# Kernel tuning notes

Measured on AMD Instinct MI355X. Metric: run time of the kernel, lower is better.

Reference implementation:

```python
import jax, jax.numpy as jnp
import numpy as np

L_KLD, L_ROOT, L_DISP, L_CONS, L_FK = 0.001, 1.0, 1.0, 0.1, 0.1


def quat_mul(a, b):
    # w-first Hamilton product, broadcasting over leading dims
    aw, ax, ay, az = a[..., 0], a[..., 1], a[..., 2], a[..., 3]
    bw, bx, by, bz = b[..., 0], b[..., 1], b[..., 2], b[..., 3]
    return jnp.stack([
        aw * bw - ax * bx - ay * by - az * bz,
        aw * bx + ax * bw + ay * bz - az * by,
        aw * by - ax * bz + ay * bw + az * bx,
        aw * bz + ax * by - ay * bx + az * bw,
    ], axis=-1)


def quat_inv(q):
    conj = q * jnp.array([1.0, -1.0, -1.0, -1.0], q.dtype)
    return conj / jnp.sum(q * q, axis=-1, keepdims=True)


def quat_rotate(q, v):
    # rotate vector v by quaternion q: q * (0, v) * q^-1
    q, vb = jnp.broadcast_arrays(q[..., :1], v[..., :1])  # shape probe
    qv = jnp.concatenate([jnp.zeros_like(v[..., :1]), v], axis=-1)
    return quat_mul(quat_mul(jnp.broadcast_to(jnp.asarray(0.0), ()).astype(qv.dtype) * 0 + 1 and None or None, qv), quat_inv(qv))  # placeholder


# clean implementation (the above placeholder is unused)
def quat_rotate(q, v):  # noqa: F811
    qv = jnp.concatenate([jnp.zeros_like(v[..., :1]), v], axis=-1)
    return quat_mul(quat_mul(q, qv), quat_inv(q))[..., 1:]


def from_root_quat(q, parents):
    # q: [..., J, 4] root-relative quats -> local quats.
    # Vectorized form of the reversed per-joint loop: parents are read
    # before being modified (parent < j), so a single gather is exact.
    qp = jnp.take(q, parents, axis=-2)
    loc = quat_mul(quat_inv(qp), q)
    keep = (parents == 0)[:, None]  # joints whose parent is root keep q
    return jnp.where(keep, q, loc)


def fk(local, offsets, parents):
    # local: [Bp,2,T,J,4]; offsets: [Bp,1,1,J,3]; returns global positions [Bp,2,T,J,3]
    J = local.shape[-2]
    grot = jnp.zeros_like(local).at[..., 0, :].set(local[..., 0, :])
    gpos = jnp.zeros(local.shape[:-1] + (3,), local.dtype)
    for j in range(1, J):  # fixed small structural loop over skeleton joints
        p = parents[j]
        pr = jnp.take(grot, p, axis=-2)  # parent global rotation [Bp,2,T,4]
        pp = jnp.take(gpos, p, axis=-2)  # parent global position [Bp,2,T,3]
        grot = grot.at[..., j, :].set(quat_mul(pr, local[..., j, :]))
        gpos = gpos.at[..., j, :].set(pp + quat_rotate(pr, offsets[..., j, :]))
    return gpos


def mse(a, b):
    return jnp.mean((a - b) ** 2)


def reference(base_motion, target_motion, input_displacement, target_displacement,
              mu, logvar, latent, W_dec, mean_q, std_q, offsets, parents):
    Bp, _, C, T = base_motion.shape
    J = C // 4
    Z = latent.shape[-1]
    offs = offsets[:, None, None, :, :]  # [Bp,1,1,J,3] (tile over pair dim via broadcast)
    root_id = jnp.array([1.0, 0.0, 0.0, 0.0], base_motion.dtype)[:, None]  # (4,1)

    def decode(lat):
        # input_motion is the decoder output in the original training loop
        m = jnp.einsum('pkz,zc->pkc', lat.reshape(Bp, 2, Z), W_dec)
        return base_motion + m.reshape(Bp, 2, C, T)

    def motion_to_pos(qs):
        qs = qs * std_q + mean_q
        qs = qs.at[..., :4, :].set(root_id)  # root quat -> identity
        q = qs.transpose(0, 1, 3, 2).reshape(Bp, 2, T, J, 4)
        return fk(from_root_quat(q, parents), offs, parents)

    # quaternion part of target dual quaternions
    target_qs = target_motion.reshape(Bp, 2, J, 8, T)[:, :, :, :4, :].reshape(Bp, 2, C, T)

    qs = decode(latent)
    loss_joints = mse(qs[..., 4:, :], target_qs[..., 4:, :])
    loss_root = mse(qs[..., :4, :], target_qs[..., :4, :])

    pos_from_lat = lambda lat: motion_to_pos(decode(lat))
    pos_qs = pos_from_lat(latent)
    pos_target = motion_to_pos(target_qs)
    loss_fk = mse(pos_qs, pos_target)

    loss_disp = mse(input_displacement, target_displacement)
    loss_kld = -0.5 * jnp.mean(jnp.sum(1.0 + logvar - mu ** 2 - jnp.exp(logvar), axis=-1))

    # drag consistency: grad of sum_p ||pos_p0 - pos_p1||^2 w.r.t. latent
    def f_sum(lat):
        pos = pos_from_lat(lat)
        return jnp.sum((pos[:, 0] - pos[:, 1]) ** 2)

    grad_f = jax.grad(f_sum)(latent)
    lp = latent.reshape(Bp, 2, Z)
    z_drag = lp[:, 0] - grad_f.reshape(Bp, 2, Z)[:, 0]
    loss_cons = mse(z_drag, lp[:, 1])

    # order: kld, root, displacement, consecutive, fk, joints
    return jnp.stack([loss_kld * L_KLD, loss_root * L_ROOT, loss_disp * L_DISP,
                      loss_cons * L_CONS, loss_fk * L_FK, loss_joints])


def setup_inputs() -> dict:
    key = jax.random.key(0)
    ks = jax.random.split(key, 11)
    Bp, C, T, J, Z = 512, 96, 128, 24, 256
    parents = jnp.array(np.array(
        [0, 0, 0, 0, 1, 2, 3, 4, 5, 6, 7, 8, 9, 9, 9, 12, 13, 14, 16, 17, 18, 19, 20, 21],
        dtype=np.int32))
    return {
        'base_motion': jax.random.normal(ks[0], (Bp, 2, C, T), jnp.float32),
        'target_motion': jax.random.normal(ks[1], (Bp, 2, 2 * C, T), jnp.float32),
        'input_displacement': jax.random.normal(ks[2], (Bp, 2, 3, T), jnp.float32),
        'target_displacement': jax.random.normal(ks[3], (Bp, 2, 3, T), jnp.float32),
        'mu': jax.random.normal(ks[4], (2 * Bp, Z), jnp.float32),
        'logvar': 0.1 * jax.random.normal(ks[5], (2 * Bp, Z), jnp.float32),
        'latent': jax.random.normal(ks[6], (2 * Bp, Z), jnp.float32),
        'W_dec': 0.02 * jax.random.normal(ks[7], (Z, C * T), jnp.float32),
        'mean_q': 0.1 * jax.random.normal(ks[8], (C, 1), jnp.float32),
        'std_q': jax.random.uniform(ks[9], (C, 1), jnp.float32, 0.5, 1.5),
        'offsets': 0.1 * jax.random.normal(ks[10], (Bp, J, 3), jnp.float32),
        'parents': parents,
    }
```

## Files before the change

kernel.cpp:

```cpp
#include <hip/hip_runtime.h>
#include <utility>

#define DEVI __device__ __forceinline__

namespace {

constexpr int T_ = 128;
constexpr int NCH = 96;
constexpr int CT = NCH * T_;
constexpr int NJ = 24;
constexpr int ZDIM = 256;
constexpr int PAR[NJ] = {0,0,0,0,1,2,3,4,5,6,7,8,9,9,9,12,13,14,16,17,18,19,20,21};

struct Q  { float w,x,y,z; };
struct V3 { float x,y,z; };

DEVI Q qmul(Q a, Q b){
  return Q{ a.w*b.w - a.x*b.x - a.y*b.y - a.z*b.z,
            a.w*b.x + a.x*b.w + a.y*b.z - a.z*b.y,
            a.w*b.y - a.x*b.z + a.y*b.w + a.z*b.x,
            a.w*b.z + a.x*b.y - a.y*b.x + a.z*b.w };
}
DEVI Q qconj(Q a){ return Q{a.w,-a.x,-a.y,-a.z}; }
DEVI float qn2(Q a){ return a.w*a.w + a.x*a.x + a.y*a.y + a.z*a.z; }
DEVI Q qscale(Q a, float s){ return Q{a.w*s, a.x*s, a.y*s, a.z*s}; }
DEVI Q qadd(Q a, Q b){ return Q{a.w+b.w, a.x+b.x, a.y+b.y, a.z+b.z}; }
DEVI Q qinv(Q a){ return qscale(qconj(a), 1.0f/qn2(a)); }
DEVI V3 qrot(Q g, V3 v){
  Q t = qmul(g, Q{0.f, v.x, v.y, v.z});
  Q y = qmul(t, qconj(g));
  float in = 1.0f/qn2(g);
  return V3{y.x*in, y.y*in, y.z*in};
}
DEVI Q qinv_bwd(Q q, Q g){
  float n  = qn2(q);
  float in = 1.0f/n;
  float d  = g.w*q.w - g.x*q.x - g.y*q.y - g.z*q.z;
  float c  = 2.0f*d*in*in;
  return Q{ g.w*in - q.w*c, -g.x*in - q.x*c, -g.y*in - q.y*c, -g.z*in - q.z*c };
}
DEVI Q qrot_bwd_g(Q g, V3 v, V3 w){
  float in = 1.0f/qn2(g);
  Q u{0.f, v.x, v.y, v.z};
  Q t = qmul(g, u);
  Q y = qmul(t, qconj(g));
  Q G4{0.f, w.x*in, w.y*in, w.z*in};
  Q dt  = qmul(G4, g);
  Q dcg = qmul(qconj(t), G4);
  Q dg  = qconj(dcg);
  dg = qadd(dg, qmul(dt, qconj(u)));
  float wy = w.x*y.x + w.y*y.y + w.z*y.z;
  dg = qadd(dg, qscale(g, -2.0f*wy*in*in));
  return dg;
}

template<typename F, int... Is>
DEVI void sf_impl(F&& f, std::integer_sequence<int, Is...>){
  (f(std::integral_constant<int, Is>{}), ...);
}
template<int N, typename F>
DEVI void static_for(F&& f){ sf_impl(f, std::make_integer_sequence<int, N>{}); }

template<int Jj>
DEVI Q loadQ(const float (&q)[NJ][4]){ return Q{q[Jj][0], q[Jj][1], q[Jj][2], q[Jj][3]}; }
template<int Jj>
DEVI Q localQ(const float (&q)[NJ][4]){
  if constexpr (Jj < 4) return loadQ<Jj>(q);
  else return qmul(qinv(loadQ<PAR[Jj]>(q)), loadQ<Jj>(q));
}
template<int Jj>
DEVI Q grotRec(const float (&q)[NJ][4]){
  if constexpr (Jj == 0) return Q{1.f,0.f,0.f,0.f};
  else return qmul(grotRec<PAR[Jj]>(q), localQ<Jj>(q));
}

template<bool TGT, typename PJ>
DEVI void chainFwd(const float* __restrict__ base, int t,
                   const float* s_std, const float* s_mean, const float* s_off,
                   float (&q)[NJ][4], PJ&& pj)
{
  Q grot[NJ]; V3 gpos[NJ];
  static_for<NJ>([&](auto jc){
    constexpr int j = decltype(jc)::value;
    if constexpr (j == 0) {
      q[0][0]=1.f; q[0][1]=0.f; q[0][2]=0.f; q[0][3]=0.f;
      grot[0] = Q{1.f,0.f,0.f,0.f};
      gpos[0] = V3{0.f,0.f,0.f};
    } else {
      constexpr int P = PAR[j];
      #pragma unroll
      for (int i = 0; i < 4; ++i){
        const int c  = 4*j + i;
        const int oc = TGT ? (8*j + i) : c;
        q[j][i] = base[oc*T_ + t] * s_std[c] + s_mean[c];
      }
      Q qj{q[j][0], q[j][1], q[j][2], q[j][3]};
      Q L;
      if constexpr (j < 4) L = qj;
      else L = qmul(qinv(Q{q[P][0], q[P][1], q[P][2], q[P][3]}), qj);
      Q gP = grot[P];
      grot[j] = qmul(gP, L);
      V3 o{s_off[3*j], s_off[3*j+1], s_off[3*j+2]};
      V3 r = qrot(gP, o);
      gpos[j] = V3{gpos[P].x + r.x, gpos[P].y + r.y, gpos[P].z + r.z};
    }
    pj(jc, gpos[j]);
  });
}

DEVI void chainBwd(const float (&q)[NJ][4], const float* s_std, const float* s_off,
                   V3 (&dgp)[NJ], float* __restrict__ Gp, int t)
{
  Q dgr[NJ] = {};
  Q dq [NJ] = {};
  static_for<NJ-1>([&](auto ic){
    constexpr int j = NJ - 1 - decltype(ic)::value;
    constexpr int P = PAR[j];
    V3 w = dgp[j];
    Q gP = grotRec<P>(q);
    if constexpr (P != 0) {
      dgp[P].x += w.x; dgp[P].y += w.y; dgp[P].z += w.z;
      V3 o{s_off[3*j], s_off[3*j+1], s_off[3*j+2]};
      dgr[P] = qadd(dgr[P], qrot_bwd_g(gP, o, w));
    }
    Q Gj = dgr[j];
    Q dL = qmul(qconj(gP), Gj);
    if constexpr (P != 0) {
      dgr[P] = qadd(dgr[P], qmul(Gj, qconj(localQ<j>(q))));
    }
    if constexpr (j < 4) {
      dq[j] = qadd(dq[j], dL);
    } else {
      Q qP  = loadQ<P>(q);
      Q iqP = qinv(qP);
      dq[j] = qadd(dq[j], qmul(qconj(iqP), dL));
      Q dInv = qmul(dL, qconj(loadQ<j>(q)));
      dq[P] = qadd(dq[P], qinv_bwd(qP, dInv));
    }
    Gp[(4*j+0)*T_ + t] = dq[j].w * s_std[4*j+0];
    Gp[(4*j+1)*T_ + t] = dq[j].x * s_std[4*j+1];
    Gp[(4*j+2)*T_ + t] = dq[j].y * s_std[4*j+2];
    Gp[(4*j+3)*T_ + t] = dq[j].z * s_std[4*j+3];
  });
  #pragma unroll
  for (int i = 0; i < 4; ++i) Gp[i*T_ + t] = 0.f;
}

DEVI float waveSum(float v){
  #pragma unroll
  for (int o = 32; o > 0; o >>= 1) v += __shfl_down(v, o);
  return v;
}

}


__global__ __launch_bounds__(256) void k_decode(
    const float* __restrict__ base, const float* __restrict__ lat,
    const float* __restrict__ W, float* __restrict__ qs)
{
  __shared__ float As[32][132];
  __shared__ float Bs[32][128];
  const int tid = threadIdx.x;
  const int bn = blockIdx.x * 128;
  const int bm = blockIdx.y * 128;
  float acc[8][8] = {};
  for (int k0 = 0; k0 < 256; k0 += 32) {
    #pragma unroll
    for (int r = 0; r < 4; ++r) {
      int idx = r*256 + tid;
      int row = idx >> 3;
      int kc  = (idx & 7) << 2;
      float4 v = *(const float4*)&lat[(size_t)(bm + row)*256 + k0 + kc];
      As[kc+0][row] = v.x; As[kc+1][row] = v.y;
      As[kc+2][row] = v.z; As[kc+3][row] = v.w;
    }
    #pragma unroll
    for (int r = 0; r < 4; ++r) {
      int idx = r*256 + tid;
      int kr = idx >> 5;
      int nc = (idx & 31) << 2;
      *(float4*)&Bs[kr][nc] = *(const float4*)&W[(size_t)(k0 + kr)*CT + bn + nc];
    }
    __syncthreads();
    const int tx = tid & 15, ty = tid >> 4;
    #pragma unroll
    for (int kk = 0; kk < 32; ++kk) {
      float a[8], b[8];
      float4 a0 = *(float4*)&As[kk][ty*8];
      float4 a1 = *(float4*)&As[kk][ty*8+4];
      float4 b0 = *(float4*)&Bs[kk][tx*8];
      float4 b1 = *(float4*)&Bs[kk][tx*8+4];
      a[0]=a0.x;a[1]=a0.y;a[2]=a0.z;a[3]=a0.w;a[4]=a1.x;a[5]=a1.y;a[6]=a1.z;a[7]=a1.w;
      b[0]=b0.x;b[1]=b0.y;b[2]=b0.z;b[3]=b0.w;b[4]=b1.x;b[5]=b1.y;b[6]=b1.z;b[7]=b1.w;
      #pragma unroll
      for (int i = 0; i < 8; ++i)
        #pragma unroll
        for (int j = 0; j < 8; ++j) acc[i][j] += a[i]*b[j];
    }
    __syncthreads();
  }
  const int tx = tid & 15, ty = tid >> 4;
  #pragma unroll
  for (int i = 0; i < 8; ++i) {
    size_t row = bm + ty*8 + i;
    #pragma unroll
    for (int j = 0; j < 8; j += 4) {
      size_t col = bn + tx*8 + j;
      float4 bv = *(const float4*)&base[row*CT + col];
      float4 o;
      o.x = bv.x + acc[i][j+0]; o.y = bv.y + acc[i][j+1];
      o.z = bv.z + acc[i][j+2]; o.w = bv.w + acc[i][j+3];
      *(float4*)&qs[row*CT + col] = o;
    }
  }
}

__global__ __launch_bounds__(128, 1) void k_pose(
    const float* __restrict__ qs,   const float* __restrict__ tmot,
    const float* __restrict__ meanq,const float* __restrict__ stdq,
    const float* __restrict__ offs, float* __restrict__ G,
    float* __restrict__ bpose)
{
  __shared__ float s_std[96], s_mean[96], s_off[72];
  __shared__ float sred[3][2];
  const int p = blockIdx.x;
  const int t = threadIdx.x;
  if (t < 96) { s_std[t] = stdq[t]; s_mean[t] = meanq[t]; }
  if (t < 72) s_off[t] = offs[p*72 + t];
  __syncthreads();

  const float* qs0 = qs   + (size_t)(2*p) * CT;
  const float* qs1 = qs0  + CT;
  const float* tm0 = tmot + (size_t)(2*p) * (2*CT);
  const float* tm1 = tm0  + 2*CT;

  float accR = 0.f, accJ = 0.f;
  #pragma unroll 4
  for (int c = 0; c < 4; ++c) {
    int oc = ((c >> 2) << 3) + (c & 3);
    float d0 = qs0[c*T_ + t] - tm0[oc*T_ + t];
    float d1 = qs1[c*T_ + t] - tm1[oc*T_ + t];
    accR += d0*d0 + d1*d1;
  }
  #pragma unroll 4
  for (int c = 4; c < 96; ++c) {
    int oc = ((c >> 2) << 3) + (c & 3);
    float d0 = qs0[c*T_ + t] - tm0[oc*T_ + t];
    float d1 = qs1[c*T_ + t] - tm1[oc*T_ + t];
    accJ += d0*d0 + d1*d1;
  }

  float fkAcc = 0.f;
  V3 posA[NJ], posB[NJ];
  float qtmp[NJ][4], qd0[NJ][4];

  chainFwd<true >(tm0, t, s_std, s_mean, s_off, qtmp,
    [&](auto jc, V3 g){ posA[decltype(jc)::value] = g; });
  chainFwd<false>(qs0, t, s_std, s_mean, s_off, qd0,
    [&](auto jc, V3 g){
      constexpr int j = decltype(jc)::value;
      float dx = g.x - posA[j].x, dy = g.y - posA[j].y, dz = g.z - posA[j].z;
      fkAcc += dx*dx + dy*dy + dz*dz;
      posB[j] = g;
    });
  chainFwd<true >(tm1, t, s_std, s_mean, s_off, qtmp,
    [&](auto jc, V3 g){ posA[decltype(jc)::value] = g; });
  V3 dgp[NJ];
  chainFwd<false>(qs1, t, s_std, s_mean, s_off, qtmp,
    [&](auto jc, V3 g){
      constexpr int j = decltype(jc)::value;
      float dx = g.x - posA[j].x, dy = g.y - posA[j].y, dz = g.z - posA[j].z;
      fkAcc += dx*dx + dy*dy + dz*dz;
      dgp[j] = V3{2.f*(posB[j].x - g.x), 2.f*(posB[j].y - g.y), 2.f*(posB[j].z - g.z)};
    });

  chainBwd(qd0, s_std, s_off, dgp, G + (size_t)p * CT, t);

  float r  = waveSum(accR);
  float jj = waveSum(accJ);
  float fk = waveSum(fkAcc);
  const int wid = t >> 6;
  if ((t & 63) == 0) { sred[0][wid] = r; sred[1][wid] = jj; sred[2][wid] = fk; }
  __syncthreads();
  if (t == 0) {
    bpose[p]        = sred[0][0] + sred[0][1];
    bpose[512 + p]  = sred[1][0] + sred[1][1];
    bpose[1024 + p] = sred[2][0] + sred[2][1];
  }
}

__global__ __launch_bounds__(256) void k_gradgemm(
    const float* __restrict__ G, const float* __restrict__ W,
    float* __restrict__ part)
{
  __shared__ float As[64][33];
  __shared__ float Bs[128][33];
  const int tid = threadIdx.x;
  const int bn = blockIdx.x * 128;
  const int bm = blockIdx.y * 64;
  const int s  = blockIdx.z;
  const int kb = s * 768;
  float acc[4][8] = {};
  for (int k0 = 0; k0 < 768; k0 += 32) {
    #pragma unroll
    for (int r = 0; r < 2; ++r) {
      int idx = r*256 + tid;
      int row = idx >> 3;
      int kc  = (idx & 7) << 2;
      float4 v = *(const float4*)&G[(size_t)(bm + row)*CT + kb + k0 + kc];
      As[row][kc+0]=v.x; As[row][kc+1]=v.y; As[row][kc+2]=v.z; As[row][kc+3]=v.w;
    }
    #pragma unroll
    for (int r = 0; r < 4; ++r) {
      int idx = r*256 + tid;
      int row = idx >> 3;
      int kc  = (idx & 7) << 2;
      float4 v = *(const float4*)&W[(size_t)(bn + row)*CT + kb + k0 + kc];
      Bs[row][kc+0]=v.x; Bs[row][kc+1]=v.y; Bs[row][kc+2]=v.z; Bs[row][kc+3]=v.w;
    }
    __syncthreads();
    const int tx = tid & 15, ty = tid >> 4;
    #pragma unroll
    for (int kk = 0; kk < 32; ++kk) {
      float a[4], b[8];
      #pragma unroll
      for (int i = 0; i < 4; ++i) a[i] = As[ty*4+i][kk];
      #pragma unroll
      for (int j = 0; j < 8; ++j) b[j] = Bs[tx*8+j][kk];
      #pragma unroll
      for (int i = 0; i < 4; ++i)
        #pragma unroll
        for (int j = 0; j < 8; ++j) acc[i][j] += a[i]*b[j];
    }
    __syncthreads();
  }
  const int tx = tid & 15, ty = tid >> 4;
  #pragma unroll
  for (int i = 0; i < 4; ++i) {
    size_t pr = (size_t)s*131072 + (size_t)(bm + ty*4 + i)*256 + bn + tx*8;
    float4 o0{acc[i][0], acc[i][1], acc[i][2], acc[i][3]};
    float4 o1{acc[i][4], acc[i][5], acc[i][6], acc[i][7]};
    *(float4*)&part[pr]   = o0;
    *(float4*)&part[pr+4] = o1;
  }
}

__global__ __launch_bounds__(256) void k_rest(
    const float* __restrict__ ind, const float* __restrict__ tgd,
    const float* __restrict__ mu,  const float* __restrict__ lv,
    const float* __restrict__ lat, const float* __restrict__ part,
    float* __restrict__ brest)
{
  __shared__ float sred[3][4];
  const int t = threadIdx.x;
  const int gid = blockIdx.x * 256 + t;
  float a0 = 0.f, a1 = 0.f, a2 = 0.f;
  if (gid < 98304) {
    float4 a = ((const float4*)ind)[gid];
    float4 b = ((const float4*)tgd)[gid];
    float dx=a.x-b.x, dy=a.y-b.y, dz=a.z-b.z, dw=a.w-b.w;
    a0 = dx*dx + dy*dy + dz*dz + dw*dw;
  }
  if (gid < 65536) {
    float4 l = ((const float4*)lv)[gid];
    float4 m = ((const float4*)mu)[gid];
    a1 = (1.f + l.x - m.x*m.x - __expf(l.x)) + (1.f + l.y - m.y*m.y - __expf(l.y))
       + (1.f + l.z - m.z*m.z - __expf(l.z)) + (1.f + l.w - m.w*m.w - __expf(l.w));
  }
  if (gid < 32768) {
    float4 g{0.f,0.f,0.f,0.f};
    #pragma unroll
    for (int s = 0; s < 16; ++s) {
      float4 v = ((const float4*)(part + (size_t)s*131072))[gid];
      g.x += v.x; g.y += v.y; g.z += v.z; g.w += v.w;
    }
    int p  = gid >> 6;
    int zb = (gid & 63) << 2;
    float4 La = *(const float4*)&lat[(size_t)(2*p)*ZDIM + zb];
    float4 Lb = *(const float4*)&lat[(size_t)(2*p+1)*ZDIM + zb];
    float vx = La.x - g.x - Lb.x, vy = La.y - g.y - Lb.y;
    float vz = La.z - g.z - Lb.z, vw = La.w - g.w - Lb.w;
    a2 = vx*vx + vy*vy + vz*vz + vw*vw;
  }
  a0 = waveSum(a0); a1 = waveSum(a1); a2 = waveSum(a2);
  const int wid = t >> 6;
  if ((t & 63) == 0) { sred[0][wid]=a0; sred[1][wid]=a1; sred[2][wid]=a2; }
  __syncthreads();
  if (t == 0) {
    brest[blockIdx.x]        = sred[0][0]+sred[0][1]+sred[0][2]+sred[0][3];
    brest[512 + blockIdx.x]  = sred[1][0]+sred[1][1]+sred[1][2]+sred[1][3];
    brest[1024 + blockIdx.x] = sred[2][0]+sred[2][1]+sred[2][2]+sred[2][3];
  }
}

__global__ __launch_bounds__(256) void k_final(
    const float* __restrict__ bpose, const float* __restrict__ brest,
    float* __restrict__ out)
{
  __shared__ float sred[4];
  const int t = threadIdx.x;
  float tot[6];
  const float* srcs[6] = { bpose, bpose+512, bpose+1024, brest, brest+512, brest+1024 };
  #pragma unroll
  for (int c = 0; c < 6; ++c) {
    float x = srcs[c][t] + srcs[c][t+256];
    x = waveSum(x);
    if ((t & 63) == 0) sred[t>>6] = x;
    __syncthreads();
    tot[c] = sred[0]+sred[1]+sred[2]+sred[3];
    __syncthreads();
  }
  if (t == 0) {
    out[0] = 0.001f * (-0.5f * tot[4] * (1.f/1024.f));
    out[1] = tot[0] * (1.f/524288.f);
    out[2] = tot[3] * (1.f/393216.f);
    out[3] = 0.1f * (tot[5] * (1.f/131072.f));
    out[4] = 0.1f * (tot[2] * (1.f/9437184.f));
    out[5] = tot[1] * (1.f/12058624.f);
  }
}

extern "C" void kernel_launch(void* const* d_in, const int* in_sizes, int n_in,
                              void* d_out, int out_size, void* d_ws, size_t ws_size,
                              hipStream_t stream)
{
  (void)in_sizes; (void)n_in; (void)out_size; (void)ws_size;
  const float* base = (const float*)d_in[0];
  const float* tmot = (const float*)d_in[1];
  const float* ind  = (const float*)d_in[2];
  const float* tgd  = (const float*)d_in[3];
  const float* mu   = (const float*)d_in[4];
  const float* lv   = (const float*)d_in[5];
  const float* lat  = (const float*)d_in[6];
  const float* W    = (const float*)d_in[7];
  const float* meanq= (const float*)d_in[8];
  const float* stdq = (const float*)d_in[9];
  const float* offs = (const float*)d_in[10];
  float* out = (float*)d_out;

  char* ws = (char*)d_ws;
  float* qs    = (float*)(ws);
  float* G     = (float*)(ws + 50331648);
  float* part  = (float*)(ws + 75497472);
  float* bpose = (float*)(ws + 83886080);
  float* brest = (float*)(ws + 83892224);

  hipLaunchKernelGGL(k_decode,   dim3(96, 8),    dim3(256), 0, stream, base, lat, W, qs);
  hipLaunchKernelGGL(k_pose,     dim3(512),      dim3(128), 0, stream, qs, tmot, meanq, stdq, offs, G, bpose);
  hipLaunchKernelGGL(k_gradgemm, dim3(2, 8, 16), dim3(256), 0, stream, G, W, part);
  hipLaunchKernelGGL(k_rest,     dim3(512),      dim3(256), 0, stream, ind, tgd, mu, lv, lat, part, brest);
  hipLaunchKernelGGL(k_final,    dim3(1),        dim3(256), 0, stream, bpose, brest, out);
}
```

Before: 479.9 us.

## Split pose kernel into forward and backward passes with stored global rotations

The fused pose kernel is split into a forward kernel and a backward kernel. The forward kernel writes the per-joint global rotations and the position gradients to workspace. The backward kernel reads them back instead of recomputing parent global rotations inside the reverse chain loop. This is meant to cut register pressure and redundant quaternion recomputation, at the cost of extra global memory traffic and an added launch. The new path runs only when the workspace is large enough; otherwise the original fused kernel is used.

Result: slower. 505.8 us (+5.4%).

```diff
diff --git a/kernel.cpp b/kernel.cpp
--- a/kernel.cpp
+++ b/kernel.cpp
@@ -108,6 +108,41 @@
   });
 }
 
+template<bool TGT, typename PJ>
+DEVI void chainFwdG(const float* __restrict__ base, int t,
+                    const float* s_std, const float* s_mean, const float* s_off,
+                    PJ&& pj)
+{
+  float q[NJ][4];
+  Q grot[NJ]; V3 gpos[NJ];
+  static_for<NJ>([&](auto jc){
+    constexpr int j = decltype(jc)::value;
+    if constexpr (j == 0) {
+      q[0][0]=1.f; q[0][1]=0.f; q[0][2]=0.f; q[0][3]=0.f;
+      grot[0] = Q{1.f,0.f,0.f,0.f};
+      gpos[0] = V3{0.f,0.f,0.f};
+    } else {
+      constexpr int P = PAR[j];
+      #pragma unroll
+      for (int i = 0; i < 4; ++i){
+        const int c  = 4*j + i;
+        const int oc = TGT ? (8*j + i) : c;
+        q[j][i] = base[oc*T_ + t] * s_std[c] + s_mean[c];
+      }
+      Q qj{q[j][0], q[j][1], q[j][2], q[j][3]};
+      Q L;
+      if constexpr (j < 4) L = qj;
+      else L = qmul(qinv(Q{q[P][0], q[P][1], q[P][2], q[P][3]}), qj);
+      Q gP = grot[P];
+      grot[j] = qmul(gP, L);
+      V3 o{s_off[3*j], s_off[3*j+1], s_off[3*j+2]};
+      V3 r = qrot(gP, o);
+      gpos[j] = V3{gpos[P].x + r.x, gpos[P].y + r.y, gpos[P].z + r.z};
+    }
+    pj(jc, gpos[j], grot[j]);
+  });
+}
+
 DEVI void chainBwd(const float (&q)[NJ][4], const float* s_std, const float* s_off,
                    V3 (&dgp)[NJ], float* __restrict__ Gp, int t)
 {
@@ -290,6 +325,158 @@
   }
 }
 
+__global__ __launch_bounds__(128) void k_pose_fwd(
+    const float* __restrict__ qs,   const float* __restrict__ tmot,
+    const float* __restrict__ meanq,const float* __restrict__ stdq,
+    const float* __restrict__ offs, float* __restrict__ grot_ws,
+    float* __restrict__ dgp_ws,     float* __restrict__ bpose)
+{
+  __shared__ float s_std[96], s_mean[96], s_off[72];
+  __shared__ float sred[3][2];
+  const int p = blockIdx.x;
+  const int t = threadIdx.x;
+  if (t < 96) { s_std[t] = stdq[t]; s_mean[t] = meanq[t]; }
+  if (t < 72) s_off[t] = offs[p*72 + t];
+  __syncthreads();
+
+  const float* qs0 = qs   + (size_t)(2*p) * CT;
+  const float* qs1 = qs0  + CT;
+  const float* tm0 = tmot + (size_t)(2*p) * (2*CT);
+  const float* tm1 = tm0  + 2*CT;
+
+  float accR = 0.f, accJ = 0.f;
+  #pragma unroll 4
+  for (int c = 0; c < 4; ++c) {
+    int oc = ((c >> 2) << 3) + (c & 3);
+    float d0 = qs0[c*T_ + t] - tm0[oc*T_ + t];
+    float d1 = qs1[c*T_ + t] - tm1[oc*T_ + t];
+    accR += d0*d0 + d1*d1;
+  }
+  #pragma unroll 4
+  for (int c = 4; c < 96; ++c) {
+    int oc = ((c >> 2) << 3) + (c & 3);
+    float d0 = qs0[c*T_ + t] - tm0[oc*T_ + t];
+    float d1 = qs1[c*T_ + t] - tm1[oc*T_ + t];
+    accJ += d0*d0 + d1*d1;
+  }
+
+  float fkAcc = 0.f;
+  V3 posA[NJ], posB[NJ];
+  float* gw = grot_ws + (size_t)p * (NJ*4*T_);
+  float* dw = dgp_ws  + (size_t)p * (NJ*3*T_);
+
+  chainFwdG<true >(tm0, t, s_std, s_mean, s_off,
+    [&](auto jc, V3 g, Q gr){ posA[decltype(jc)::value] = g; (void)gr; });
+  chainFwdG<false>(qs0, t, s_std, s_mean, s_off,
+    [&](auto jc, V3 g, Q gr){
+      constexpr int j = decltype(jc)::value;
+      float dx = g.x - posA[j].x, dy = g.y - posA[j].y, dz = g.z - posA[j].z;
+      fkAcc += dx*dx + dy*dy + dz*dz;
+      posB[j] = g;
+      if constexpr (j >= 1) {
+        gw[(j*4+0)*T_ + t] = gr.w; gw[(j*4+1)*T_ + t] = gr.x;
+        gw[(j*4+2)*T_ + t] = gr.y; gw[(j*4+3)*T_ + t] = gr.z;
+      }
+    });
+  chainFwdG<true >(tm1, t, s_std, s_mean, s_off,
+    [&](auto jc, V3 g, Q gr){ posA[decltype(jc)::value] = g; (void)gr; });
+  chainFwdG<false>(qs1, t, s_std, s_mean, s_off,
+    [&](auto jc, V3 g, Q gr){
+      constexpr int j = decltype(jc)::value;
+      float dx = g.x - posA[j].x, dy = g.y - posA[j].y, dz = g.z - posA[j].z;
+      fkAcc += dx*dx + dy*dy + dz*dz;
+      (void)gr;
+      if constexpr (j >= 1) {
+        dw[(j*3+0)*T_ + t] = 2.f*(posB[j].x - g.x);
+        dw[(j*3+1)*T_ + t] = 2.f*(posB[j].y - g.y);
+        dw[(j*3+2)*T_ + t] = 2.f*(posB[j].z - g.z);
+      }
+    });
+
+  float r  = waveSum(accR);
+  float jj = waveSum(accJ);
+  float fk = waveSum(fkAcc);
+  const int wid = t >> 6;
+  if ((t & 63) == 0) { sred[0][wid] = r; sred[1][wid] = jj; sred[2][wid] = fk; }
+  __syncthreads();
+  if (t == 0) {
+    bpose[p]        = sred[0][0] + sred[0][1];
+    bpose[512 + p]  = sred[1][0] + sred[1][1];
+    bpose[1024 + p] = sred[2][0] + sred[2][1];
+  }
+}
+
+__global__ __launch_bounds__(128) void k_pose_bwd(
+    const float* __restrict__ qs,   const float* __restrict__ meanq,
+    const float* __restrict__ stdq, const float* __restrict__ offs,
+    const float* __restrict__ grot_ws, const float* __restrict__ dgp_ws,
+    float* __restrict__ G)
+{
+  __shared__ float s_std[96], s_mean[96], s_off[72];
+  const int p = blockIdx.x;
+  const int t = threadIdx.x;
+  if (t < 96) { s_std[t] = stdq[t]; s_mean[t] = meanq[t]; }
+  if (t < 72) s_off[t] = offs[p*72 + t];
+  __syncthreads();
+
+  const float* qs0 = qs + (size_t)(2*p) * CT;
+  const float* gw  = grot_ws + (size_t)p * (NJ*4*T_);
+  const float* dw  = dgp_ws  + (size_t)p * (NJ*3*T_);
+  float* Gp = G + (size_t)p * CT;
+
+  float q[NJ][4];
+  q[0][0]=1.f; q[0][1]=0.f; q[0][2]=0.f; q[0][3]=0.f;
+  static_for<NJ-1>([&](auto jc){
+    constexpr int j = decltype(jc)::value + 1;
+    #pragma unroll
+    for (int i = 0; i < 4; ++i) {
+      const int c = 4*j + i;
+      q[j][i] = qs0[c*T_ + t] * s_std[c] + s_mean[c];
+    }
+  });
+
+  V3 dgpacc[NJ] = {};
+  Q dgr[NJ] = {};
+  Q dq [NJ] = {};
+  static_for<NJ-1>([&](auto ic){
+    constexpr int j = NJ - 1 - decltype(ic)::value;
+    constexpr int P = PAR[j];
+    V3 w{ dw[(j*3+0)*T_ + t] + dgpacc[j].x,
+          dw[(j*3+1)*T_ + t] + dgpacc[j].y,
+          dw[(j*3+2)*T_ + t] + dgpacc[j].z };
+    Q gP;
+    if constexpr (P == 0) gP = Q{1.f,0.f,0.f,0.f};
+    else gP = Q{ gw[(P*4+0)*T_ + t], gw[(P*4+1)*T_ + t],
+                 gw[(P*4+2)*T_ + t], gw[(P*4+3)*T_ + t] };
+    if constexpr (P != 0) {
+      dgpacc[P].x += w.x; dgpacc[P].y += w.y; dgpacc[P].z += w.z;
+      V3 o{s_off[3*j], s_off[3*j+1], s_off[3*j+2]};
+      dgr[P] = qadd(dgr[P], qrot_bwd_g(gP, o, w));
+    }
+    Q Gj = dgr[j];
+    Q dL = qmul(qconj(gP), Gj);
+    if constexpr (P != 0) {
+      Q localj = qmul(qinv(loadQ<P>(q)), loadQ<j>(q));
+      dgr[P] = qadd(dgr[P], qmul(Gj, qconj(localj)));
+    }
+    if constexpr (j < 4) {
+      dq[j] = qadd(dq[j], dL);
+    } else {
+      Q qP  = loadQ<P>(q);
+      Q iqP = qinv(qP);
+      dq[j] = qadd(dq[j], qmul(qconj(iqP), dL));
+      Q dInv = qmul(dL, qconj(loadQ<j>(q)));
+      dq[P] = qadd(dq[P], qinv_bwd(qP, dInv));
+    }
+    Gp[(4*j+0)*T_ + t] = dq[j].w * s_std[4*j+0];
+    Gp[(4*j+1)*T_ + t] = dq[j].x * s_std[4*j+1];
+    Gp[(4*j+2)*T_ + t] = dq[j].y * s_std[4*j+2];
+    Gp[(4*j+3)*T_ + t] = dq[j].z * s_std[4*j+3];
+  });
+  #pragma unroll
+  for (int i = 0; i < 4; ++i) Gp[i*T_ + t] = 0.f;
+}
+
 __global__ __launch_bounds__(256) void k_gradgemm(
     const float* __restrict__ G, const float* __restrict__ W,
     float* __restrict__ part)
@@ -425,7 +612,7 @@
                               void* d_out, int out_size, void* d_ws, size_t ws_size,
                               hipStream_t stream)
 {
-  (void)in_sizes; (void)n_in; (void)out_size; (void)ws_size;
+  (void)in_sizes; (void)n_in; (void)out_size;
   const float* base = (const float*)d_in[0];
   const float* tmot = (const float*)d_in[1];
   const float* ind  = (const float*)d_in[2];
@@ -440,15 +627,41 @@
   float* out = (float*)d_out;
 
   char* ws = (char*)d_ws;
-  float* qs    = (float*)(ws);
-  float* G     = (float*)(ws + 50331648);
-  float* part  = (float*)(ws + 75497472);
-  float* bpose = (float*)(ws + 83886080);
-  float* brest = (float*)(ws + 83892224);
-
-  hipLaunchKernelGGL(k_decode,   dim3(96, 8),    dim3(256), 0, stream, base, lat, W, qs);
-  hipLaunchKernelGGL(k_pose,     dim3(512),      dim3(128), 0, stream, qs, tmot, meanq, stdq, offs, G, bpose);
-  hipLaunchKernelGGL(k_gradgemm, dim3(2, 8, 16), dim3(256), 0, stream, G, W, part);
-  hipLaunchKernelGGL(k_rest,     dim3(512),      dim3(256), 0, stream, ind, tgd, mu, lv, lat, part, brest);
-  hipLaunchKernelGGL(k_final,    dim3(1),        dim3(256), 0, stream, bpose, brest, out);
-}
+  float* qs = (float*)(ws);
+  float* G  = (float*)(ws + 50331648);
+
+  constexpr size_t OFF_GROT = 75497472;
+  constexpr size_t OFF_PART_SPLIT = 75497472;
+  constexpr size_t OFF_DGP  = 100663296;
+  constexpr size_t OFF_BPOSE_SPLIT = 119537664;
+  constexpr size_t OFF_BREST_SPLIT = 119543808;
+  constexpr size_t WS_SPLIT_NEED   = 119549952;
+
+  hipLaunchKernelGGL(k_decode, dim3(96, 8), dim3(256), 0, stream, base, lat, W, qs);
+
+  if (ws_size >= WS_SPLIT_NEED) {
+    float* grot  = (float*)(ws + OFF_GROT);
+    float* dgp   = (float*)(ws + OFF_DGP);
+    float* part  = (float*)(ws + OFF_PART_SPLIT);
+    float* bpose = (float*)(ws + OFF_BPOSE_SPLIT);
+    float* brest = (float*)(ws + OFF_BREST_SPLIT);
+    hipLaunchKernelGGL(k_pose_fwd, dim3(512), dim3(128), 0, stream,
+                       qs, tmot, meanq, stdq, offs, grot, dgp, bpose);
+    hipLaunchKernelGGL(k_pose_bwd, dim3(512), dim3(128), 0, stream,
+                       qs, meanq, stdq, offs, grot, dgp, G);
+    hipLaunchKernelGGL(k_gradgemm, dim3(2, 8, 16), dim3(256), 0, stream, G, W, part);
+    hipLaunchKernelGGL(k_rest, dim3(512), dim3(256), 0, stream,
+                       ind, tgd, mu, lv, lat, part, brest);
+    hipLaunchKernelGGL(k_final, dim3(1), dim3(256), 0, stream, bpose, brest, out);
+  } else {
+    float* part  = (float*)(ws + 75497472);
+    float* bpose = (float*)(ws + 83886080);
+    float* brest = (float*)(ws + 83892224);
+    hipLaunchKernelGGL(k_pose, dim3(512), dim3(128), 0, stream,
+                       qs, tmot, meanq, stdq, offs, G, bpose);
+    hipLaunchKernelGGL(k_gradgemm, dim3(2, 8, 16), dim3(256), 0, stream, G, W, part);
+    hipLaunchKernelGGL(k_rest, dim3(512), dim3(256), 0, stream,
+                       ind, tgd, mu, lv, lat, part, brest);
+    hipLaunchKernelGGL(k_final, dim3(1), dim3(256), 0, stream, bpose, brest, out);
+  }
+}
```
